# Optimization experiments

Hardware: AMD Instinct MI355X
Metric: run time of the kernel (lower is better)

Reference implementation:

```python
import jax, jax.numpy as jnp
import numpy as np

# Static problem sizes (uniform ragged batch -> dense-packable)
B, NC, NP, C = 16, 128, 256, 128
HID = 2 * C            # mlp_hidden_scale * embedding_channels
COORD_SCALE = 5.0      # args.coord_scale
DIS_THRES = 10.0       # args.dis_map_thres
N_PROT = 16384         # total protein_whole residues
MAXN = 2 + NC + NP     # per-sample complex length (glb_c + compound + glb_p + pocket)


def setup_inputs() -> dict:
    key = jax.random.key(0)
    ks = jax.random.split(key, 12)
    protein_feats = jax.random.normal(ks[0], (N_PROT, 1280), jnp.float32)
    compound_feats = jax.random.normal(ks[1], (B * NC, 56), jnp.float32)
    complex_coords = jax.random.normal(ks[2], (B * MAXN, 3), jnp.float32) * 10.0
    dis_map = jax.random.uniform(ks[3], (B * NP * NC,), jnp.float32) * DIS_THRES
    keep_idx = jnp.sort(jax.random.randint(ks[4], (B * NP,), 0, N_PROT))
    glb_c = jnp.ones((1, C), jnp.float32)
    glb_p = jnp.ones((1, C), jnp.float32)
    # xavier_uniform with gain=0.001 ~ tiny weights
    W_prot = jax.random.normal(ks[5], (1280, C), jnp.float32) * 0.001
    b_prot = jnp.zeros((C,), jnp.float32)
    W_comp = jax.random.normal(ks[6], (56, C), jnp.float32) * 0.001
    b_comp = jnp.zeros((C,), jnp.float32)
    W1 = jax.random.normal(ks[7], (C, HID), jnp.float32) / np.sqrt(C)
    b1 = jnp.zeros((HID,), jnp.float32)
    W2 = jax.random.normal(ks[8], (HID, 1), jnp.float32) / np.sqrt(HID)
    b2 = jnp.zeros((1,), jnp.float32)
    return dict(protein_feats=protein_feats, compound_feats=compound_feats,
                complex_coords=complex_coords, dis_map=dis_map, keep_idx=keep_idx,
                glb_c=glb_c, glb_p=glb_p, W_prot=W_prot, b_prot=b_prot,
                W_comp=W_comp, b_comp=b_comp, W1=W1, b1=b1, W2=W2, b2=b2)


def reference(protein_feats, compound_feats, complex_coords, dis_map, keep_idx,
              glb_c, glb_p, W_prot, b_prot, W_comp, b_comp, W1, b1, W2, b2):
    # --- input projections + keepNode gather (pocket residues from whole protein)
    pocket_emb = (protein_feats[keep_idx] @ W_prot + b_prot).reshape(B, NP, C)
    compound_emb = (compound_feats @ W_comp + b_comp).reshape(B, NC, C)

    # --- ragged batch assembly: per-sample [glb_c, compound_i, glb_p, pocket_i]
    # (uniform sizes -> single dense concat replaces the Python loop of mask+cat)
    gc = jnp.broadcast_to(glb_c[None], (B, 1, C))
    gp = jnp.broadcast_to(glb_p[None], (B, 1, C))
    new_samples = jnp.concatenate([gc, compound_emb, gp, pocket_emb], axis=1)  # [B, MAXN, C]

    # --- stand-in pair embedding for EfficientMCAttModel output:
    # pair_embed_batched[b, i, j] over (glb_p+pocket) x (glb_c+compound)
    p_side = new_samples[:, NC + 1:, :]     # [B, NP+1, C]
    c_side = new_samples[:, :NC + 1, :]     # [B, NC+1, C]
    pair = p_side[:, :, None, :] + c_side[:, None, :, :]  # [B, NP+1, NC+1, C]

    # --- coordinates (normalize, split by segment/is_global layout)
    coords = (complex_coords / COORD_SCALE).reshape(B, MAXN, 3)
    compound_coords_n = coords[:, 1:NC + 1, :]   # [B, NC, 3]
    pocket_coords_n = coords[:, NC + 2:, :]      # [B, NP, 3]

    # --- cdist(pocket, compound)  [B, NP, NC]
    diff = pocket_coords_n[:, :, None, :] - compound_coords_n[:, None, :, :]
    dmap = jnp.sqrt(jnp.sum(diff * diff, axis=-1) + 1e-12)

    # --- distmap MLP on z = pair[:, 1:, 1:] then sigmoid * thres
    z = pair[:, 1:, 1:, :]                        # [B, NP, NC, C]
    h = jax.nn.relu(z @ W1 + b1)                  # [B, NP, NC, HID]
    logits = (h @ W2 + b2)[..., 0]                # [B, NP, NC]
    # z_mask = outer(pocket_mask, compound_mask) is all-True for uniform sizes
    y_pred = jax.nn.sigmoid(logits).reshape(-1) * DIS_THRES
    y_pred_by_coords = jnp.clip(dmap.reshape(-1) * COORD_SCALE, 0.0, DIS_THRES)

    compound_coords_out = compound_coords_n.reshape(-1, 3) * COORD_SCALE
    pocket_coords_out = pocket_coords_n.reshape(-1, 3) * COORD_SCALE
    compound_batch = jnp.repeat(jnp.arange(B, dtype=jnp.int32), NC)
    pocket_batch = jnp.repeat(jnp.arange(B, dtype=jnp.int32), NP)
    keepNode_less_5 = jnp.zeros((), jnp.int32)
    return (compound_coords_out, compound_batch, pocket_coords_out, pocket_batch,
            y_pred, y_pred_by_coords, dis_map, keepNode_less_5)
```

## Files before the change

### kernel.cpp

```cpp
#include <hip/hip_runtime.h>
#include <hip/hip_bf16.h>
#include <cstddef>


typedef __attribute__((ext_vector_type(8))) short short8v;
typedef __attribute__((ext_vector_type(4))) float f32x4;
typedef _Float16 half2v __attribute__((ext_vector_type(2)));
typedef _Float16 half8v __attribute__((ext_vector_type(8)));

__device__ __forceinline__ unsigned int f2bf(float x) {
    unsigned int u = __float_as_uint(x);
    return (u + 0x7fffu + ((u >> 16) & 1u)) >> 16;
}

__device__ __forceinline__ float dot8h(half8v r, half8v w, float acc) {
#if __has_builtin(__builtin_amdgcn_fdot2)
#pragma unroll
    for (int q = 0; q < 4; ++q) {
        half2v rq = {r[2 * q], r[2 * q + 1]};
        half2v wq = {w[2 * q], w[2 * q + 1]};
        acc = __builtin_amdgcn_fdot2(rq, wq, acc, false);
    }
#else
#pragma unroll
    for (int q = 0; q < 8; ++q) acc += (float)r[q] * (float)w[q];
#endif
    return acc;
}

#define WS_WTP   0u
#define WS_WTC   655360u
#define WS_BP1   688128u
#define WS_BC1   689152u
#define WS_W2H   690176u
#define WS_P1H   691200u
#define WS_PP0   3836928u
#define WS_PP1   8031232u

__global__ __launch_bounds__(256) void k_fusew(const float* __restrict__ Wp,
                                               const float* __restrict__ Wc,
                                               const float* __restrict__ bp,
                                               const float* __restrict__ bc,
                                               const float* __restrict__ W1,
                                               const float* __restrict__ b1,
                                               const float* __restrict__ W2,
                                               char* __restrict__ ws) {
    __shared__ float Al[8][128];
    const int tid = threadIdx.x, bid = blockIdx.x;
    const int row0 = bid * 8;
    {
        const int r = tid >> 5, k4 = (tid & 31) * 4;
        const int rg = row0 + r;
        float4 v = make_float4(0.f, 0.f, 0.f, 0.f);
        if (rg < 1280)       v = *reinterpret_cast<const float4*>(Wp + (size_t)rg * 128 + k4);
        else if (rg < 1336)  v = *reinterpret_cast<const float4*>(Wc + (size_t)(rg - 1280) * 128 + k4);
        else if (rg == 1336) v = *reinterpret_cast<const float4*>(bp + k4);
        else if (rg == 1337) v = *reinterpret_cast<const float4*>(bc + k4);
        *reinterpret_cast<float4*>(&Al[r][k4]) = v;
    }
    __syncthreads();
    float acc[8];
#pragma unroll
    for (int r = 0; r < 8; ++r) acc[r] = 0.f;
#pragma unroll 4
    for (int k4 = 0; k4 < 128; k4 += 4) {
        float w0 = W1[(k4 + 0) * 256 + tid];
        float w1 = W1[(k4 + 1) * 256 + tid];
        float w2 = W1[(k4 + 2) * 256 + tid];
        float w3 = W1[(k4 + 3) * 256 + tid];
#pragma unroll
        for (int r = 0; r < 8; ++r) {
            float4 a = *reinterpret_cast<const float4*>(&Al[r][k4]);
            acc[r] += a.x * w0 + a.y * w1 + a.z * w2 + a.w * w3;
        }
    }
    if (bid < 160) {
        unsigned int w[4];
#pragma unroll
        for (int q = 0; q < 4; ++q)
            w[q] = f2bf(acc[2 * q]) | (f2bf(acc[2 * q + 1]) << 16);
        unsigned short* WtP = (unsigned short*)(ws + WS_WTP);
        *reinterpret_cast<uint4*>(WtP + (size_t)tid * 1280 + row0) = make_uint4(w[0], w[1], w[2], w[3]);
    } else if (bid < 167) {
        unsigned int w[4];
#pragma unroll
        for (int q = 0; q < 4; ++q)
            w[q] = f2bf(acc[2 * q]) | (f2bf(acc[2 * q + 1]) << 16);
        unsigned short* WtC = (unsigned short*)(ws + WS_WTC);
        *reinterpret_cast<uint4*>(WtC + (size_t)tid * 64 + (row0 - 1280)) = make_uint4(w[0], w[1], w[2], w[3]);
    } else {
        ((float*)(ws + WS_BP1))[tid] = acc[0] + b1[tid];
        ((float*)(ws + WS_BC1))[tid] = acc[1];
        ((_Float16*)(ws + WS_W2H))[tid] = (_Float16)W2[tid];
        unsigned short* WtC = (unsigned short*)(ws + WS_WTC);
        *reinterpret_cast<uint4*>(WtC + (size_t)tid * 64 + 56) = make_uint4(0, 0, 0, 0);
    }
}

struct AB { float4 ra[2]; uint4 rb[8]; };

__device__ __forceinline__ void load_tile(AB& t, bool pocket, int koff,
                                          const float* __restrict__ prot,
                                          const float* __restrict__ comp,
                                          const int* keepL, int m0,
                                          const unsigned short* __restrict__ Bt,
                                          int bstride, int tid) {
#pragma unroll
    for (int u = 0; u < 2; ++u) {
        const int unit = tid + 256 * u;
        const int r = unit >> 4, kc = unit & 15;
        float4 v = make_float4(0.f, 0.f, 0.f, 0.f);
        if (pocket) {
            v = *reinterpret_cast<const float4*>(prot + (size_t)keepL[r] * 1280 + koff + kc * 4);
        } else if (kc < 14) {
            v = *reinterpret_cast<const float4*>(comp + (size_t)(m0 + r - 4096) * 56 + kc * 4);
        }
        t.ra[u] = v;
    }
#pragma unroll
    for (int u = 0; u < 8; ++u) {
        const int unit = tid + 256 * u;
        const int col = unit >> 3, k8 = unit & 7;
        t.rb[u] = *reinterpret_cast<const uint4*>(Bt + (size_t)col * bstride + koff + k8 * 8);
    }
}

__device__ __forceinline__ void store_tile(const AB& t, char* As, char* Bs, int tid) {
#pragma unroll
    for (int u = 0; u < 2; ++u) {
        const int unit = tid + 256 * u;
        const int r = unit >> 4, kc = unit & 15;
        const float4 v = t.ra[u];
        const unsigned int lo = f2bf(v.x) | (f2bf(v.y) << 16);
        const unsigned int hi = f2bf(v.z) | (f2bf(v.w) << 16);
        const int wb = (r * 128 + kc * 8) ^ ((r & 7) << 4);
        *reinterpret_cast<uint2*>(As + wb) = make_uint2(lo, hi);
    }
#pragma unroll
    for (int u = 0; u < 8; ++u) {
        const int unit = tid + 256 * u;
        const int col = unit >> 3, k8 = unit & 7;
        const int wb = (col * 128 + k8 * 16) ^ ((col & 7) << 4);
        *reinterpret_cast<uint4*>(Bs + wb) = t.rb[u];
    }
}

__global__ __launch_bounds__(256) void k_gemm(const float* __restrict__ prot,
                                              const int* __restrict__ keep,
                                              const float* __restrict__ comp,
                                              char* __restrict__ ws) {
    __shared__ __align__(16) char As[32 * 64 * 2];
    __shared__ __align__(16) char Bs[256 * 64 * 2];
    __shared__ int keepL[32];
    const int tid = threadIdx.x;
    const int l = tid & 63, wn = tid >> 6;
    const int l15 = l & 15, lg = l >> 4;
    const int bid = blockIdx.x;
    const bool pocket = (bid < 256);
    const int ks = pocket ? (bid & 1) : 0;
    const int m0 = pocket ? ((bid >> 1) * 32) : (4096 + (bid - 256) * 32);
    const int koff0 = ks * 640;
    const int iters = pocket ? 10 : 1;
    const unsigned short* Bt = (const unsigned short*)(ws + (pocket ? WS_WTP : WS_WTC));
    const int bstride = pocket ? 1280 : 64;

    if (pocket && tid < 32) keepL[tid] = keep[m0 + tid];
    __syncthreads();

    f32x4 acc[2][4];
#pragma unroll
    for (int m = 0; m < 2; ++m)
#pragma unroll
        for (int n = 0; n < 4; ++n) acc[m][n] = (f32x4){0.f, 0.f, 0.f, 0.f};

    AB cur, nxt;
    load_tile(cur, pocket, koff0, prot, comp, keepL, m0, Bt, bstride, tid);

    for (int it = 0; it < iters; ++it) {
        if (it) __syncthreads();
        store_tile(cur, As, Bs, tid);
        __syncthreads();
        if (it + 1 < iters)
            load_tile(nxt, pocket, koff0 + (it + 1) * 64, prot, comp, keepL, m0, Bt, bstride, tid);
#pragma unroll
        for (int kstep = 0; kstep < 2; ++kstep) {
            const int kbyte = kstep * 64 + lg * 16;
            short8v a[2], b[4];
#pragma unroll
            for (int m = 0; m < 2; ++m) {
                const int row = m * 16 + l15;
                a[m] = *reinterpret_cast<const short8v*>(As + ((row * 128 + kbyte) ^ ((row & 7) << 4)));
            }
#pragma unroll
            for (int n = 0; n < 4; ++n) {
                const int col = wn * 64 + n * 16 + l15;
                b[n] = *reinterpret_cast<const short8v*>(Bs + ((col * 128 + kbyte) ^ ((col & 7) << 4)));
            }
#pragma unroll
            for (int m = 0; m < 2; ++m)
#pragma unroll
                for (int n = 0; n < 4; ++n)
                    acc[m][n] = __builtin_amdgcn_mfma_f32_16x16x32_bf16(a[m], b[n], acc[m][n], 0, 0, 0);
        }
        if (it + 1 < iters) cur = nxt;
    }

    if (pocket) {
        float* dst = (float*)(ws + (ks ? WS_PP1 : WS_PP0));
        const float* bias = (const float*)(ws + WS_BP1);
#pragma unroll
        for (int m = 0; m < 2; ++m)
#pragma unroll
            for (int n = 0; n < 4; ++n) {
                const int col = wn * 64 + n * 16 + l15;
                const float bb = (ks == 0) ? bias[col] : 0.f;
#pragma unroll
                for (int i = 0; i < 4; ++i) {
                    const int row = m0 + m * 16 + lg * 4 + i;
                    dst[((size_t)row << 8) + col] = acc[m][n][i] + bb;
                }
            }
    } else {
        const float* bias = (const float*)(ws + WS_BC1);
        _Float16* P1h = (_Float16*)(ws + WS_P1H);
#pragma unroll
        for (int m = 0; m < 2; ++m)
#pragma unroll
            for (int n = 0; n < 4; ++n) {
                const int col = wn * 64 + n * 16 + l15;
                const float bb = bias[col];
#pragma unroll
                for (int i = 0; i < 4; ++i) {
                    const int row = m0 + m * 16 + lg * 4 + i;
                    P1h[(size_t)row * 256 + col] = (_Float16)(acc[m][n][i] + bb);
                }
            }
    }
}

__global__ __launch_bounds__(256) void k_pair(const char* __restrict__ ws,
                                              const float* __restrict__ b2,
                                              const float* __restrict__ coords,
                                              const float* __restrict__ dism,
                                              float* __restrict__ out) {
    __shared__ __align__(16) char Ph[32 * 512];
    __shared__ __align__(16) char Ch[64 * 512];
    __shared__ __align__(16) _Float16 W2l[256];
    __shared__ float pcs[32][3], ccs[64][3];
    const int tid = threadIdx.x;
    const int b = blockIdx.z, p0 = blockIdx.y * 32, c0 = blockIdx.x * 64;
    const _Float16* P1h = (const _Float16*)(ws + WS_P1H);
    const float* pp0 = (const float*)(ws + WS_PP0);
    const float* pp1 = (const float*)(ws + WS_PP1);

#pragma unroll
    for (int u = 0; u < 4; ++u) {
        const int unit = tid + 256 * u;
        const int row = unit >> 5, h8 = unit & 31;
        const size_t base = (((size_t)(b * 256 + p0 + row)) << 8) + h8 * 8;
        const float4 q0 = *reinterpret_cast<const float4*>(pp0 + base);
        const float4 q1 = *reinterpret_cast<const float4*>(pp0 + base + 4);
        const float4 r0 = *reinterpret_cast<const float4*>(pp1 + base);
        const float4 r1 = *reinterpret_cast<const float4*>(pp1 + base + 4);
        union { _Float16 h[8]; uint4 v; } U;
        U.h[0] = (_Float16)(q0.x + r0.x); U.h[1] = (_Float16)(q0.y + r0.y);
        U.h[2] = (_Float16)(q0.z + r0.z); U.h[3] = (_Float16)(q0.w + r0.w);
        U.h[4] = (_Float16)(q1.x + r1.x); U.h[5] = (_Float16)(q1.y + r1.y);
        U.h[6] = (_Float16)(q1.z + r1.z); U.h[7] = (_Float16)(q1.w + r1.w);
        const int key = ((row ^ (row >> 2)) & 7) << 4;
        *reinterpret_cast<uint4*>(Ph + ((row * 512 + h8 * 16) ^ key)) = U.v;
    }
#pragma unroll
    for (int u = 0; u < 8; ++u) {
        const int unit = tid + 256 * u;
        const int row = unit >> 5, h8 = unit & 31;
        const uint4 v = *reinterpret_cast<const uint4*>(P1h + (size_t)(4096 + b * 128 + c0 + row) * 256 + h8 * 8);
        const int key = ((row ^ (row >> 2)) & 7) << 4;
        *reinterpret_cast<uint4*>(Ch + ((row * 512 + h8 * 16) ^ key)) = v;
    }
    if (tid < 32) {
        *reinterpret_cast<uint4*>(W2l + tid * 8) =
            *reinterpret_cast<const uint4*>((const _Float16*)(ws + WS_W2H) + tid * 8);
        const float* s = coords + (size_t)(b * 386 + 130 + p0 + tid) * 3;
        pcs[tid][0] = s[0] / 5.0f; pcs[tid][1] = s[1] / 5.0f; pcs[tid][2] = s[2] / 5.0f;
    } else if (tid < 96) {
        const int t = tid - 32;
        const float* s = coords + (size_t)(b * 386 + 1 + c0 + t) * 3;
        ccs[t][0] = s[0] / 5.0f; ccs[t][1] = s[1] / 5.0f; ccs[t][2] = s[2] / 5.0f;
    }
    __syncthreads();

    const int pi = tid >> 4, ci = tid & 15;
    float acc[2][4] = {{0.f, 0.f, 0.f, 0.f}, {0.f, 0.f, 0.f, 0.f}};
#pragma unroll 4
    for (int h8 = 0; h8 < 32; ++h8) {
        const half8v wv = *reinterpret_cast<const half8v*>((const char*)W2l + h8 * 16);
        half8v pf[2], cf[4];
#pragma unroll
        for (int i = 0; i < 2; ++i) {
            const int row = pi * 2 + i;
            const int key = ((row ^ (row >> 2)) & 7) << 4;
            pf[i] = *reinterpret_cast<const half8v*>(Ph + ((row * 512 + h8 * 16) ^ key));
        }
#pragma unroll
        for (int j = 0; j < 4; ++j) {
            const int row = ci * 4 + j;
            const int key = ((row ^ (row >> 2)) & 7) << 4;
            cf[j] = *reinterpret_cast<const half8v*>(Ch + ((row * 512 + h8 * 16) ^ key));
        }
#pragma unroll
        for (int i = 0; i < 2; ++i)
#pragma unroll
            for (int j = 0; j < 4; ++j) {
                half8v s = pf[i] + cf[j];
                half8v r = __builtin_elementwise_max(s, (half8v)0);
                acc[i][j] = dot8h(r, wv, acc[i][j]);
            }
    }

    const float bb = b2[0];
#pragma unroll
    for (int i = 0; i < 2; ++i) {
        const int pr = pi * 2 + i;
        float4 y4, yc4;
        float* yp = &y4.x; float* yq = &yc4.x;
#pragma unroll
        for (int j = 0; j < 4; ++j) {
            const int cr = ci * 4 + j;
            const float logit = acc[i][j] + bb;
            yp[j] = 10.0f / (1.0f + expf(-logit));
            const float dx = pcs[pr][0] - ccs[cr][0];
            const float dy = pcs[pr][1] - ccs[cr][1];
            const float dz = pcs[pr][2] - ccs[cr][2];
            const float d = sqrtf(dx * dx + dy * dy + dz * dz + 1e-12f);
            yq[j] = fminf(fmaxf(d * 5.0f, 0.0f), 10.0f);
        }
        const size_t o = (size_t)(b * 256 + p0 + pr) * 128 + c0 + ci * 4;
        *reinterpret_cast<float4*>(out + 24576 + o) = y4;
        *reinterpret_cast<float4*>(out + 548864 + o) = yc4;
    }

    const int fb = blockIdx.x + 2 * (blockIdx.y + 8 * blockIdx.z);
    const int g = fb * 256 + tid;
    {
        const float4* src = reinterpret_cast<const float4*>(dism + (size_t)g * 8);
        float4* dst = reinterpret_cast<float4*>(out + 1073152 + (size_t)g * 8);
        dst[0] = src[0]; dst[1] = src[1];
    }
    if (g < 6144) {
        const int row = g / 3, d = g - row * 3;
        const int bb2 = row >> 7, c = row & 127;
        const float x = coords[(size_t)(bb2 * 386 + 1 + c) * 3 + d];
        out[g] = (x / 5.0f) * 5.0f;
    }
    if (g < 2048) out[6144 + g] = (float)(g >> 7);
    if (g < 12288) {
        const int row = g / 3, d = g - row * 3;
        const int bb2 = row >> 8, p = row & 255;
        const float x = coords[(size_t)(bb2 * 386 + 130 + p) * 3 + d];
        out[8192 + g] = (x / 5.0f) * 5.0f;
    }
    if (g < 4096) out[20480 + g] = (float)(g >> 8);
    if (g == 0) out[1597440] = 0.0f;
}

extern "C" void kernel_launch(void* const* d_in, const int* in_sizes, int n_in,
                              void* d_out, int out_size, void* d_ws, size_t ws_size,
                              hipStream_t stream) {
    const float* prot   = (const float*)d_in[0];
    const float* comp   = (const float*)d_in[1];
    const float* coords = (const float*)d_in[2];
    const float* dism   = (const float*)d_in[3];
    const int*   keep   = (const int*)d_in[4];
    const float* Wp = (const float*)d_in[7];
    const float* bp = (const float*)d_in[8];
    const float* Wc = (const float*)d_in[9];
    const float* bc = (const float*)d_in[10];
    const float* W1 = (const float*)d_in[11];
    const float* b1 = (const float*)d_in[12];
    const float* W2 = (const float*)d_in[13];
    const float* b2 = (const float*)d_in[14];
    float* out = (float*)d_out;
    char* ws = (char*)d_ws;

    k_fusew<<<168, 256, 0, stream>>>(Wp, Wc, bp, bc, W1, b1, W2, ws);
    k_gemm<<<320, 256, 0, stream>>>(prot, keep, comp, ws);
    k_pair<<<dim3(2, 8, 16), 256, 0, stream>>>(ws, b2, coords, dism, out);
}
```

Before: 48.34 us.

## Split pocket GEMM 4-way in K with fp16 partials, halve pair tiles, move copies

The pocket projection GEMM is split four ways along K instead of two, so it launches 576 blocks instead of 320, and its partial sums are stored as fp16 instead of fp32, which cuts workspace traffic. The pair kernel now uses 32x32 tiles instead of 32x64, doubling its grid to 512 blocks, and sums four fp16 partials with vector adds. The passthrough copy of dis_map and the coordinate and batch outputs move into extra blocks of the first weight-fusion kernel, taking them off the pair kernel's critical path. In exchange, fp16 partial sums lose some precision, and each pair block reuses loaded data less.

```diff
diff --git a/kernel.cpp b/kernel.cpp
--- a/kernel.cpp
+++ b/kernel.cpp
@@ -34,8 +34,7 @@
 #define WS_BC1   689152u
 #define WS_W2H   690176u
 #define WS_P1H   691200u
-#define WS_PP0   3836928u
-#define WS_PP1   8031232u
+#define WS_PPH   3836928u
 
 __global__ __launch_bounds__(256) void k_fusew(const float* __restrict__ Wp,
                                                const float* __restrict__ Wc,
@@ -44,9 +43,38 @@
                                                const float* __restrict__ W1,
                                                const float* __restrict__ b1,
                                                const float* __restrict__ W2,
+                                               const float* __restrict__ coords,
+                                               const float* __restrict__ dism,
+                                               float* __restrict__ out,
                                                char* __restrict__ ws) {
+    const int tid = threadIdx.x, bid = blockIdx.x;
+
+    if (bid >= 168) {
+        const int g = (bid - 168) * 256 + tid;
+        {
+            const float4* src = reinterpret_cast<const float4*>(dism + (size_t)g * 8);
+            float4* dst = reinterpret_cast<float4*>(out + 1073152 + (size_t)g * 8);
+            dst[0] = src[0]; dst[1] = src[1];
+        }
+        if (g < 6144) {
+            const int row = g / 3, d = g - row * 3;
+            const int bb2 = row >> 7, c = row & 127;
+            const float x = coords[(size_t)(bb2 * 386 + 1 + c) * 3 + d];
+            out[g] = (x / 5.0f) * 5.0f;
+        }
+        if (g < 2048) out[6144 + g] = (float)(g >> 7);
+        if (g < 12288) {
+            const int row = g / 3, d = g - row * 3;
+            const int bb2 = row >> 8, p = row & 255;
+            const float x = coords[(size_t)(bb2 * 386 + 130 + p) * 3 + d];
+            out[8192 + g] = (x / 5.0f) * 5.0f;
+        }
+        if (g < 4096) out[20480 + g] = (float)(g >> 8);
+        if (g == 0) out[1597440] = 0.0f;
+        return;
+    }
+
     __shared__ float Al[8][128];
-    const int tid = threadIdx.x, bid = blockIdx.x;
     const int row0 = bid * 8;
     {
         const int r = tid >> 5, k4 = (tid & 31) * 4;
@@ -156,11 +184,11 @@
     const int l = tid & 63, wn = tid >> 6;
     const int l15 = l & 15, lg = l >> 4;
     const int bid = blockIdx.x;
-    const bool pocket = (bid < 256);
-    const int ks = pocket ? (bid & 1) : 0;
-    const int m0 = pocket ? ((bid >> 1) * 32) : (4096 + (bid - 256) * 32);
-    const int koff0 = ks * 640;
-    const int iters = pocket ? 10 : 1;
+    const bool pocket = (bid < 512);
+    const int ks = pocket ? (bid & 3) : 0;
+    const int m0 = pocket ? ((bid >> 2) * 32) : (4096 + (bid - 512) * 32);
+    const int koff0 = ks * 320;
+    const int iters = pocket ? 5 : 1;
     const unsigned short* Bt = (const unsigned short*)(ws + (pocket ? WS_WTP : WS_WTC));
     const int bstride = pocket ? 1280 : 64;
 
@@ -206,7 +234,7 @@
     }
 
     if (pocket) {
-        float* dst = (float*)(ws + (ks ? WS_PP1 : WS_PP0));
+        _Float16* dst = (_Float16*)(ws + WS_PPH + (size_t)ks * 2097152u);
         const float* bias = (const float*)(ws + WS_BP1);
 #pragma unroll
         for (int m = 0; m < 2; ++m)
@@ -217,7 +245,7 @@
 #pragma unroll
                 for (int i = 0; i < 4; ++i) {
                     const int row = m0 + m * 16 + lg * 4 + i;
-                    dst[((size_t)row << 8) + col] = acc[m][n][i] + bb;
+                    dst[((size_t)row << 8) + col] = (_Float16)(acc[m][n][i] + bb);
                 }
             }
     } else {
@@ -241,37 +269,31 @@
 __global__ __launch_bounds__(256) void k_pair(const char* __restrict__ ws,
                                               const float* __restrict__ b2,
                                               const float* __restrict__ coords,
-                                              const float* __restrict__ dism,
                                               float* __restrict__ out) {
     __shared__ __align__(16) char Ph[32 * 512];
-    __shared__ __align__(16) char Ch[64 * 512];
+    __shared__ __align__(16) char Ch[32 * 512];
     __shared__ __align__(16) _Float16 W2l[256];
-    __shared__ float pcs[32][3], ccs[64][3];
+    __shared__ float pcs[32][3], ccs[32][3];
     const int tid = threadIdx.x;
-    const int b = blockIdx.z, p0 = blockIdx.y * 32, c0 = blockIdx.x * 64;
+    const int b = blockIdx.z, p0 = blockIdx.y * 32, c0 = blockIdx.x * 32;
     const _Float16* P1h = (const _Float16*)(ws + WS_P1H);
-    const float* pp0 = (const float*)(ws + WS_PP0);
-    const float* pp1 = (const float*)(ws + WS_PP1);
+    const _Float16* pp = (const _Float16*)(ws + WS_PPH);
 
 #pragma unroll
     for (int u = 0; u < 4; ++u) {
         const int unit = tid + 256 * u;
         const int row = unit >> 5, h8 = unit & 31;
         const size_t base = (((size_t)(b * 256 + p0 + row)) << 8) + h8 * 8;
-        const float4 q0 = *reinterpret_cast<const float4*>(pp0 + base);
-        const float4 q1 = *reinterpret_cast<const float4*>(pp0 + base + 4);
-        const float4 r0 = *reinterpret_cast<const float4*>(pp1 + base);
-        const float4 r1 = *reinterpret_cast<const float4*>(pp1 + base + 4);
-        union { _Float16 h[8]; uint4 v; } U;
-        U.h[0] = (_Float16)(q0.x + r0.x); U.h[1] = (_Float16)(q0.y + r0.y);
-        U.h[2] = (_Float16)(q0.z + r0.z); U.h[3] = (_Float16)(q0.w + r0.w);
-        U.h[4] = (_Float16)(q1.x + r1.x); U.h[5] = (_Float16)(q1.y + r1.y);
-        U.h[6] = (_Float16)(q1.z + r1.z); U.h[7] = (_Float16)(q1.w + r1.w);
+        const half8v s0 = *reinterpret_cast<const half8v*>(pp + base);
+        const half8v s1 = *reinterpret_cast<const half8v*>(pp + 1048576u + base);
+        const half8v s2 = *reinterpret_cast<const half8v*>(pp + 2097152u + base);
+        const half8v s3 = *reinterpret_cast<const half8v*>(pp + 3145728u + base);
+        const half8v t = (s0 + s1) + (s2 + s3);
         const int key = ((row ^ (row >> 2)) & 7) << 4;
-        *reinterpret_cast<uint4*>(Ph + ((row * 512 + h8 * 16) ^ key)) = U.v;
-    }
-#pragma unroll
-    for (int u = 0; u < 8; ++u) {
+        *reinterpret_cast<half8v*>(Ph + ((row * 512 + h8 * 16) ^ key)) = t;
+    }
+#pragma unroll
+    for (int u = 0; u < 4; ++u) {
         const int unit = tid + 256 * u;
         const int row = unit >> 5, h8 = unit & 31;
         const uint4 v = *reinterpret_cast<const uint4*>(P1h + (size_t)(4096 + b * 128 + c0 + row) * 256 + h8 * 8);
@@ -283,7 +305,7 @@
             *reinterpret_cast<const uint4*>((const _Float16*)(ws + WS_W2H) + tid * 8);
         const float* s = coords + (size_t)(b * 386 + 130 + p0 + tid) * 3;
         pcs[tid][0] = s[0] / 5.0f; pcs[tid][1] = s[1] / 5.0f; pcs[tid][2] = s[2] / 5.0f;
-    } else if (tid < 96) {
+    } else if (tid < 64) {
         const int t = tid - 32;
         const float* s = coords + (size_t)(b * 386 + 1 + c0 + t) * 3;
         ccs[t][0] = s[0] / 5.0f; ccs[t][1] = s[1] / 5.0f; ccs[t][2] = s[2] / 5.0f;
@@ -291,11 +313,11 @@
     __syncthreads();
 
     const int pi = tid >> 4, ci = tid & 15;
-    float acc[2][4] = {{0.f, 0.f, 0.f, 0.f}, {0.f, 0.f, 0.f, 0.f}};
+    float acc[2][2] = {{0.f, 0.f}, {0.f, 0.f}};
 #pragma unroll 4
     for (int h8 = 0; h8 < 32; ++h8) {
         const half8v wv = *reinterpret_cast<const half8v*>((const char*)W2l + h8 * 16);
-        half8v pf[2], cf[4];
+        half8v pf[2], cf[2];
 #pragma unroll
         for (int i = 0; i < 2; ++i) {
             const int row = pi * 2 + i;
@@ -303,15 +325,15 @@
             pf[i] = *reinterpret_cast<const half8v*>(Ph + ((row * 512 + h8 * 16) ^ key));
         }
 #pragma unroll
-        for (int j = 0; j < 4; ++j) {
-            const int row = ci * 4 + j;
+        for (int j = 0; j < 2; ++j) {
+            const int row = ci * 2 + j;
             const int key = ((row ^ (row >> 2)) & 7) << 4;
             cf[j] = *reinterpret_cast<const half8v*>(Ch + ((row * 512 + h8 * 16) ^ key));
         }
 #pragma unroll
         for (int i = 0; i < 2; ++i)
 #pragma unroll
-            for (int j = 0; j < 4; ++j) {
+            for (int j = 0; j < 2; ++j) {
                 half8v s = pf[i] + cf[j];
                 half8v r = __builtin_elementwise_max(s, (half8v)0);
                 acc[i][j] = dot8h(r, wv, acc[i][j]);
@@ -322,11 +344,11 @@
 #pragma unroll
     for (int i = 0; i < 2; ++i) {
         const int pr = pi * 2 + i;
-        float4 y4, yc4;
-        float* yp = &y4.x; float* yq = &yc4.x;
-#pragma unroll
-        for (int j = 0; j < 4; ++j) {
-            const int cr = ci * 4 + j;
+        float2 y2, yc2;
+        float* yp = &y2.x; float* yq = &yc2.x;
+#pragma unroll
+        for (int j = 0; j < 2; ++j) {
+            const int cr = ci * 2 + j;
             const float logit = acc[i][j] + bb;
             yp[j] = 10.0f / (1.0f + expf(-logit));
             const float dx = pcs[pr][0] - ccs[cr][0];
@@ -335,33 +357,10 @@
             const float d = sqrtf(dx * dx + dy * dy + dz * dz + 1e-12f);
             yq[j] = fminf(fmaxf(d * 5.0f, 0.0f), 10.0f);
         }
-        const size_t o = (size_t)(b * 256 + p0 + pr) * 128 + c0 + ci * 4;
-        *reinterpret_cast<float4*>(out + 24576 + o) = y4;
-        *reinterpret_cast<float4*>(out + 548864 + o) = yc4;
-    }
-
-    const int fb = blockIdx.x + 2 * (blockIdx.y + 8 * blockIdx.z);
-    const int g = fb * 256 + tid;
-    {
-        const float4* src = reinterpret_cast<const float4*>(dism + (size_t)g * 8);
-        float4* dst = reinterpret_cast<float4*>(out + 1073152 + (size_t)g * 8);
-        dst[0] = src[0]; dst[1] = src[1];
-    }
-    if (g < 6144) {
-        const int row = g / 3, d = g - row * 3;
-        const int bb2 = row >> 7, c = row & 127;
-        const float x = coords[(size_t)(bb2 * 386 + 1 + c) * 3 + d];
-        out[g] = (x / 5.0f) * 5.0f;
-    }
-    if (g < 2048) out[6144 + g] = (float)(g >> 7);
-    if (g < 12288) {
-        const int row = g / 3, d = g - row * 3;
-        const int bb2 = row >> 8, p = row & 255;
-        const float x = coords[(size_t)(bb2 * 386 + 130 + p) * 3 + d];
-        out[8192 + g] = (x / 5.0f) * 5.0f;
-    }
-    if (g < 4096) out[20480 + g] = (float)(g >> 8);
-    if (g == 0) out[1597440] = 0.0f;
+        const size_t o = (size_t)(b * 256 + p0 + pr) * 128 + c0 + ci * 2;
+        *reinterpret_cast<float2*>(out + 24576 + o) = y2;
+        *reinterpret_cast<float2*>(out + 548864 + o) = yc2;
+    }
 }
 
 extern "C" void kernel_launch(void* const* d_in, const int* in_sizes, int n_in,
@@ -383,7 +382,7 @@
     float* out = (float*)d_out;
     char* ws = (char*)d_ws;
 
-    k_fusew<<<168, 256, 0, stream>>>(Wp, Wc, bp, bc, W1, b1, W2, ws);
-    k_gemm<<<320, 256, 0, stream>>>(prot, keep, comp, ws);
-    k_pair<<<dim3(2, 8, 16), 256, 0, stream>>>(ws, b2, coords, dism, out);
-}
+    k_fusew<<<424, 256, 0, stream>>>(Wp, Wc, bp, bc, W1, b1, W2, coords, dism, out, ws);
+    k_gemm<<<576, 256, 0, stream>>>(prot, keep, comp, ws);
+    k_pair<<<dim3(4, 8, 16), 256, 0, stream>>>(ws, b2, coords, out);
+}
```

New measurement: 43.83 us. 1.1x faster.
